# Kernel optimization log

Hardware: AMD Instinct MI355X
Metric: run time of the kernel (lower is better)

The kernel has to match this reference:

```python
import jax, jax.numpy as jnp
import numpy as np

D_MODEL = 256
D_FFN = 1024
N_LEVELS = 4
N_HEADS = 8
N_POINTS = 4
HEAD_DIM = D_MODEL // N_HEADS
SPATIAL = [(128, 128), (64, 64), (32, 32), (16, 16)]
LQ = sum(h * w for h, w in SPATIAL)  # 21760
B = 2


def setup_inputs() -> dict:
    key = jax.random.key(0)
    ks = jax.random.split(key, 24)

    def w(k, shape, s=0.02):
        return (jax.random.normal(k, shape) * s).astype(jnp.float32)

    HLP = N_HEADS * N_LEVELS * N_POINTS
    starts = np.cumsum([0] + [h * w_ for h, w_ in SPATIAL[:-1]])
    return {
        "src": jax.random.normal(ks[0], (B, LQ, D_MODEL), jnp.float32),
        "pos": 0.1 * jax.random.normal(ks[1], (B, LQ, D_MODEL), jnp.float32),
        "reference_points": jax.random.uniform(ks[2], (B, LQ, N_LEVELS, 2), jnp.float32),
        "W_off": w(ks[3], (D_MODEL, HLP * 2)),
        "b_off": w(ks[4], (HLP * 2,), 0.5),
        "W_attn": w(ks[5], (D_MODEL, HLP)),
        "b_attn": jnp.zeros((HLP,), jnp.float32),
        "W_val": w(ks[6], (D_MODEL, D_MODEL)),
        "b_val": jnp.zeros((D_MODEL,), jnp.float32),
        "W_out": w(ks[7], (D_MODEL, D_MODEL)),
        "b_out": jnp.zeros((D_MODEL,), jnp.float32),
        "ln1_g": jnp.ones((D_MODEL,), jnp.float32),
        "ln1_b": jnp.zeros((D_MODEL,), jnp.float32),
        "W1": w(ks[8], (D_MODEL, D_FFN)),
        "b1": jnp.zeros((D_FFN,), jnp.float32),
        "W2": w(ks[9], (D_FFN, D_MODEL)),
        "b2": jnp.zeros((D_MODEL,), jnp.float32),
        "ln2_g": jnp.ones((D_MODEL,), jnp.float32),
        "ln2_b": jnp.zeros((D_MODEL,), jnp.float32),
        "spatial_shapes": np.array(SPATIAL, np.int32),
        "level_start_index": np.array(starts, np.int32),
    }


def _layernorm(x, g, b):
    mu = x.mean(-1, keepdims=True)
    var = ((x - mu) ** 2).mean(-1, keepdims=True)
    return (x - mu) * jax.lax.rsqrt(var + 1e-5) * g + b


def _bilinear_sample(v, x, y, H, W):
    # v: [N, H, W, D]; x, y: [N, Lq, P] pixel coords (align_corners=False, zero pad)
    x0f = jnp.floor(x)
    y0f = jnp.floor(y)
    x0 = x0f.astype(jnp.int32)
    y0 = y0f.astype(jnp.int32)
    wx1 = x - x0f
    wy1 = y - y0f
    wx0 = 1.0 - wx1
    wy0 = 1.0 - wy1
    vf = v.reshape(v.shape[0], H * W, v.shape[-1])

    def gather(xi, yi, wt):
        valid = (xi >= 0) & (xi < W) & (yi >= 0) & (yi < H)
        idx = jnp.clip(yi, 0, H - 1) * W + jnp.clip(xi, 0, W - 1)
        g = jnp.take_along_axis(vf, idx.reshape(idx.shape[0], -1)[..., None], axis=1)
        g = g.reshape(*xi.shape, vf.shape[-1])
        return g * (wt * valid.astype(wt.dtype))[..., None]

    return (gather(x0, y0, wx0 * wy0) + gather(x0 + 1, y0, wx1 * wy0)
            + gather(x0, y0 + 1, wx0 * wy1) + gather(x0 + 1, y0 + 1, wx1 * wy1))


def _ms_deform_attn(query, src, reference_points, W_off, b_off, W_attn, b_attn,
                    W_val, b_val, W_out, b_out, spatial_shapes):
    Bq, Lq, _ = query.shape
    ss = np.asarray(spatial_shapes)
    value = (src @ W_val + b_val).reshape(Bq, Lq, N_HEADS, HEAD_DIM)
    off = (query @ W_off + b_off).reshape(Bq, Lq, N_HEADS, N_LEVELS, N_POINTS, 2)
    attn = (query @ W_attn + b_attn).reshape(Bq, Lq, N_HEADS, N_LEVELS * N_POINTS)
    attn = jax.nn.softmax(attn, axis=-1).reshape(Bq, Lq, N_HEADS, N_LEVELS, N_POINTS)
    # offset normalizer = (W, H) per level
    normalizer = jnp.asarray(ss[:, ::-1].astype(np.float32))  # [L, 2]
    loc = reference_points[:, :, None, :, None, :] + off / normalizer[None, None, None, :, None, :]
    # loc: [B, Lq, M, L, P, 2] normalized in [0,1]
    out = jnp.zeros((Bq, N_HEADS, Lq, HEAD_DIM), query.dtype)
    start = 0
    for lvl in range(N_LEVELS):
        H, W = int(ss[lvl, 0]), int(ss[lvl, 1])
        v = value[:, start:start + H * W]                                 # [B, HW, M, D]
        v = v.transpose(0, 2, 1, 3).reshape(Bq * N_HEADS, H, W, HEAD_DIM)
        l = loc[:, :, :, lvl]                                             # [B, Lq, M, P, 2]
        x = (l[..., 0] * W - 0.5).transpose(0, 2, 1, 3).reshape(Bq * N_HEADS, Lq, N_POINTS)
        y = (l[..., 1] * H - 0.5).transpose(0, 2, 1, 3).reshape(Bq * N_HEADS, Lq, N_POINTS)
        sampled = _bilinear_sample(v, x, y, H, W)                         # [BM, Lq, P, D]
        wgt = attn[:, :, :, lvl].transpose(0, 2, 1, 3).reshape(Bq * N_HEADS, Lq, N_POINTS)
        out = out + (sampled * wgt[..., None]).sum(2).reshape(Bq, N_HEADS, Lq, HEAD_DIM)
        start += H * W
    out = out.transpose(0, 2, 1, 3).reshape(Bq, Lq, D_MODEL)
    return out @ W_out + b_out


def reference(src, pos, reference_points, W_off, b_off, W_attn, b_attn, W_val, b_val,
              W_out, b_out, ln1_g, ln1_b, W1, b1, W2, b2, ln2_g, ln2_b,
              spatial_shapes, level_start_index):
    query = src + pos
    src2 = _ms_deform_attn(query, src, reference_points, W_off, b_off, W_attn, b_attn,
                           W_val, b_val, W_out, b_out, spatial_shapes)
    h = _layernorm(src + src2, ln1_g, ln1_b)
    ffn = jax.nn.relu(h @ W1 + b1) @ W2 + b2
    return _layernorm(h + ffn, ln2_g, ln2_b)
```

## Files before the change

### kernel.cpp

```cpp
#include <hip/hip_runtime.h>

typedef __bf16 bf16x8 __attribute__((ext_vector_type(8)));
typedef float f32x4 __attribute__((ext_vector_type(4)));

static constexpr int TOKS = 43520;
static constexpr int LQN  = 21760;

__device__ __forceinline__ unsigned short f2bf(float f) {
  union { float f; unsigned u; } v; v.f = f;
  return (unsigned short)((v.u + 0x7fffu + ((v.u >> 16) & 1u)) >> 16);
}
__device__ __forceinline__ float bf2f(unsigned short b) {
  union { unsigned u; float f; } v; v.u = ((unsigned)b) << 16; return v.f;
}

__global__ __launch_bounds__(256) void prewt_kernel(
    const float* __restrict__ src, const float* __restrict__ pos,
    unsigned short* __restrict__ srcb, unsigned short* __restrict__ qb,
    const float* __restrict__ W_val, const float* __restrict__ W_off,
    const float* __restrict__ W_attn, const float* __restrict__ W_out,
    const float* __restrict__ W1, const float* __restrict__ W2,
    const float* __restrict__ b_off, const float* __restrict__ b_attn,
    unsigned short* __restrict__ Wt_val, unsigned short* __restrict__ Wt_oa,
    unsigned short* __restrict__ Wt_out,
    unsigned short* __restrict__ Wt_1, unsigned short* __restrict__ Wt_2,
    float* __restrict__ b_oa) {
  const int bid = blockIdx.x;
  if (bid < 10880) {
    int i = bid * 256 + threadIdx.x;
    float4 s = ((const float4*)src)[i], p = ((const float4*)pos)[i];
    ((ushort4*)srcb)[i] = make_ushort4(f2bf(s.x), f2bf(s.y), f2bf(s.z), f2bf(s.w));
    ((ushort4*)qb)[i]   = make_ushort4(f2bf(s.x + p.x), f2bf(s.y + p.y),
                                       f2bf(s.z + p.z), f2bf(s.w + p.w));
    return;
  }
  int gid = (bid - 10880) * 256 + threadIdx.x;
  if (gid >= 754048) return;
  if (gid >= 753664) {
    int i = gid - 753664;
    b_oa[i] = (i < 256) ? b_off[i] : b_attn[i - 256];
    return;
  }
  const float* W; unsigned short* Wt; int idx, K, nsh;
  if (gid < 65536)       { W = W_val;  Wt = Wt_val;          idx = gid;          K = 256;  nsh = 8;  }
  else if (gid < 131072) { W = W_off;  Wt = Wt_oa;           idx = gid - 65536;  K = 256;  nsh = 8;  }
  else if (gid < 163840) { W = W_attn; Wt = Wt_oa + 65536;   idx = gid - 131072; K = 256;  nsh = 7;  }
  else if (gid < 229376) { W = W_out;  Wt = Wt_out;          idx = gid - 163840; K = 256;  nsh = 8;  }
  else if (gid < 491520) { W = W1;     Wt = Wt_1;            idx = gid - 229376; K = 256;  nsh = 10; }
  else                   { W = W2;     Wt = Wt_2;            idx = gid - 491520; K = 1024; nsh = 8;  }
  int k = idx >> nsh, n = idx & ((1 << nsh) - 1);
  Wt[n * K + k] = f2bf(W[idx]);
}

template <int K, int OUTOP>
__device__ __forceinline__ void gemm_body(unsigned short* __restrict__ As,
                                          unsigned short* __restrict__ Bs,
                                          const unsigned short* __restrict__ A,
                                          const unsigned short* __restrict__ Bt,
                                          const float* __restrict__ bias,
                                          const unsigned short* __restrict__ res,
                                          unsigned short* __restrict__ Cp,
                                          int N, int bm, int bn) {
  const int t = threadIdx.x;
  const int wave = t >> 6, lane = t & 63;
  const int wm = (wave & 1) << 6, wn = (wave >> 1) << 6;
  const int lr = lane & 15, lq = lane >> 4;
  const int row0 = t >> 2, cb0 = (t & 3) << 3;
  f32x4 acc[4][4] = {};
  const unsigned short* ga = A  + (size_t)(bm * 128 + row0) * K + cb0;
  const unsigned short* gb = Bt + (size_t)(bn * 128 + row0) * K + cb0;
  const size_t gs = (size_t)64 * K;
  uint4 pa0 = *(const uint4*)ga;
  uint4 pa1 = *(const uint4*)(ga + gs);
  uint4 pb0 = *(const uint4*)gb;
  uint4 pb1 = *(const uint4*)(gb + gs);
  int p = 0;
#pragma unroll 1
  for (int k0 = 0; k0 < K; k0 += 32) {
    unsigned short* Ab = As + p * 5120;
    unsigned short* Bb = Bs + p * 5120;
    *(uint4*)&Ab[row0 * 40 + cb0] = pa0;
    *(uint4*)&Ab[(row0 + 64) * 40 + cb0] = pa1;
    *(uint4*)&Bb[row0 * 40 + cb0] = pb0;
    *(uint4*)&Bb[(row0 + 64) * 40 + cb0] = pb1;
    __syncthreads();
    if (k0 + 32 < K) {
      pa0 = *(const uint4*)(ga + k0 + 32);
      pa1 = *(const uint4*)(ga + gs + k0 + 32);
      pb0 = *(const uint4*)(gb + k0 + 32);
      pb1 = *(const uint4*)(gb + gs + k0 + 32);
    }
    bf16x8 af[4], bfr[4];
#pragma unroll
    for (int i = 0; i < 4; i++) af[i] = *(const bf16x8*)&Ab[(wm + i * 16 + lr) * 40 + lq * 8];
#pragma unroll
    for (int j = 0; j < 4; j++) bfr[j] = *(const bf16x8*)&Bb[(wn + j * 16 + lr) * 40 + lq * 8];
#pragma unroll
    for (int i = 0; i < 4; i++)
#pragma unroll
      for (int j = 0; j < 4; j++)
        acc[i][j] = __builtin_amdgcn_mfma_f32_16x16x32_bf16(af[i], bfr[j], acc[i][j], 0, 0, 0);
    p ^= 1;
  }
  const int rb = bm * 128 + wm + lq * 4;
  const int cbase = bn * 128 + wn + lr;
#pragma unroll
  for (int j = 0; j < 4; j++) {
    const int col = cbase + j * 16;
    const float bv = bias[col];
#pragma unroll
    for (int i = 0; i < 4; i++) {
#pragma unroll
      for (int r = 0; r < 4; r++) {
        float v = acc[i][j][r] + bv;
        size_t o = (size_t)(rb + i * 16 + r) * N + col;
        if (OUTOP == 1) Cp[o] = f2bf(v);
        else if (OUTOP == 2) Cp[o] = f2bf(fmaxf(v, 0.f));
        else Cp[o] = f2bf(v + bf2f(res[o]));
      }
    }
  }
}

__global__ __launch_bounds__(256) void proj_kernel(
    const unsigned short* __restrict__ srcb, const unsigned short* __restrict__ qb,
    const unsigned short* __restrict__ Wt_val, const unsigned short* __restrict__ Wt_oa,
    const float* __restrict__ b_val, const float* __restrict__ b_oa,
    unsigned short* __restrict__ valb, unsigned short* __restrict__ oab) {
  __shared__ unsigned short As[2 * 5120];
  __shared__ unsigned short Bs[2 * 5120];
  const int bn = blockIdx.y;
  if (bn < 2)
    gemm_body<256, 1>(As, Bs, srcb, Wt_val, b_val, nullptr, valb, 256, blockIdx.x, bn);
  else
    gemm_body<256, 1>(As, Bs, qb, Wt_oa, b_oa, nullptr, oab, 384, blockIdx.x, bn - 2);
}

template <int K, int MODE>
__device__ __forceinline__ void big_body(unsigned short* __restrict__ As,
                                         unsigned short* __restrict__ Bs,
                                         const unsigned short* __restrict__ A,
                                         const unsigned short* __restrict__ Bt,
                                         const float* __restrict__ bias,
                                         const unsigned short* __restrict__ res,
                                         const float* __restrict__ gamma,
                                         const float* __restrict__ beta,
                                         void* __restrict__ outp,
                                         int N, int bm, int bn) {
  const int t = threadIdx.x;
  const int wave = t >> 6, lane = t & 63;
  const int wm = (wave & 1) << 6, wn = (wave >> 1) << 7;
  const int lr = lane & 15, lq = lane >> 4;
  const int row0 = t >> 2, cb0 = (t & 3) << 3;
  f32x4 acc[4][8] = {};
  const unsigned short* ga = A  + (size_t)(bm * 128 + row0) * K + cb0;
  const unsigned short* gb = Bt + (size_t)(bn * 256 + row0) * K + cb0;
  const size_t gs = (size_t)64 * K;
  uint4 pa0 = *(const uint4*)ga;
  uint4 pa1 = *(const uint4*)(ga + gs);
  uint4 pb0 = *(const uint4*)gb;
  uint4 pb1 = *(const uint4*)(gb + gs);
  uint4 pb2 = *(const uint4*)(gb + 2 * gs);
  uint4 pb3 = *(const uint4*)(gb + 3 * gs);
  int p = 0;
#pragma unroll 1
  for (int k0 = 0; k0 < K; k0 += 32) {
    unsigned short* Ab = As + p * 5120;
    unsigned short* Bb = Bs + p * 10240;
    *(uint4*)&Ab[row0 * 40 + cb0] = pa0;
    *(uint4*)&Ab[(row0 + 64) * 40 + cb0] = pa1;
    *(uint4*)&Bb[row0 * 40 + cb0] = pb0;
    *(uint4*)&Bb[(row0 + 64) * 40 + cb0] = pb1;
    *(uint4*)&Bb[(row0 + 128) * 40 + cb0] = pb2;
    *(uint4*)&Bb[(row0 + 192) * 40 + cb0] = pb3;
    __syncthreads();
    if (k0 + 32 < K) {
      pa0 = *(const uint4*)(ga + k0 + 32);
      pa1 = *(const uint4*)(ga + gs + k0 + 32);
      pb0 = *(const uint4*)(gb + k0 + 32);
      pb1 = *(const uint4*)(gb + gs + k0 + 32);
      pb2 = *(const uint4*)(gb + 2 * gs + k0 + 32);
      pb3 = *(const uint4*)(gb + 3 * gs + k0 + 32);
    }
    bf16x8 af[4], bfr[8];
#pragma unroll
    for (int i = 0; i < 4; i++) af[i]  = *(const bf16x8*)&Ab[(wm + i * 16 + lr) * 40 + lq * 8];
#pragma unroll
    for (int j = 0; j < 8; j++) bfr[j] = *(const bf16x8*)&Bb[(wn + j * 16 + lr) * 40 + lq * 8];
#pragma unroll
    for (int i = 0; i < 4; i++)
#pragma unroll
      for (int j = 0; j < 8; j++)
        acc[i][j] = __builtin_amdgcn_mfma_f32_16x16x32_bf16(af[i], bfr[j], acc[i][j], 0, 0, 0);
    p ^= 1;
  }
  const int rb = bm * 128 + wm + lq * 4;
  if (MODE == 0) {
    const int cbase = bn * 256 + wn + lr;
#pragma unroll
    for (int j = 0; j < 8; j++) {
      const int col = cbase + j * 16;
      const float bv = bias[col];
#pragma unroll
      for (int i = 0; i < 4; i++)
#pragma unroll
        for (int r = 0; r < 4; r++) {
          float v = acc[i][j][r] + bv;
          ((unsigned short*)outp)[(size_t)(rb + i * 16 + r) * N + col] = f2bf(fmaxf(v, 0.f));
        }
    }
    return;
  }
  __syncthreads();
  float* red = (float*)As;
  const int wnIdx = wave >> 1;
  float vsum[4][4], vsq[4][4];
#pragma unroll
  for (int i = 0; i < 4; i++)
#pragma unroll
    for (int r = 0; r < 4; r++) { vsum[i][r] = 0.f; vsq[i][r] = 0.f; }
#pragma unroll
  for (int j = 0; j < 8; j++) {
    const int col = wn + j * 16 + lr;
    const float bv = bias[col];
#pragma unroll
    for (int i = 0; i < 4; i++)
#pragma unroll
      for (int r = 0; r < 4; r++) {
        const int grow = rb + i * 16 + r;
        float v = acc[i][j][r] + bv + bf2f(res[(size_t)grow * 256 + col]);
        acc[i][j][r] = v;
        vsum[i][r] += v;
        vsq[i][r]  += v * v;
      }
  }
#pragma unroll
  for (int m = 1; m <= 8; m <<= 1)
#pragma unroll
    for (int i = 0; i < 4; i++)
#pragma unroll
      for (int r = 0; r < 4; r++) {
        vsum[i][r] += __shfl_xor(vsum[i][r], m, 64);
        vsq[i][r]  += __shfl_xor(vsq[i][r],  m, 64);
      }
  if (lr == 0) {
#pragma unroll
    for (int i = 0; i < 4; i++)
#pragma unroll
      for (int r = 0; r < 4; r++) {
        const int lrow = wm + i * 16 + lq * 4 + r;
        red[wnIdx * 128 + lrow]       = vsum[i][r];
        red[256 + wnIdx * 128 + lrow] = vsq[i][r];
      }
  }
  __syncthreads();
  float mu[4][4], rstd[4][4];
#pragma unroll
  for (int i = 0; i < 4; i++)
#pragma unroll
    for (int r = 0; r < 4; r++) {
      const int lrow = wm + i * 16 + lq * 4 + r;
      const float ts = vsum[i][r] + red[(1 - wnIdx) * 128 + lrow];
      const float tq = vsq[i][r]  + red[256 + (1 - wnIdx) * 128 + lrow];
      const float m_ = ts * (1.f / 256.f);
      float var = tq * (1.f / 256.f) - m_ * m_;
      mu[i][r] = m_;
      rstd[i][r] = rsqrtf(var + 1e-5f);
    }
#pragma unroll
  for (int j = 0; j < 8; j++) {
    const int col = wn + j * 16 + lr;
    const float gg = gamma[col], bb = beta[col];
#pragma unroll
    for (int i = 0; i < 4; i++)
#pragma unroll
      for (int r = 0; r < 4; r++) {
        const int grow = rb + i * 16 + r;
        const float y = (acc[i][j][r] - mu[i][r]) * rstd[i][r] * gg + bb;
        if (MODE == 1) ((unsigned short*)outp)[(size_t)grow * 256 + col] = f2bf(y);
        else           ((float*)outp)[(size_t)grow * 256 + col] = y;
      }
  }
}

__global__ __launch_bounds__(256, 2) void out_ln_kernel(
    const unsigned short* __restrict__ A, const unsigned short* __restrict__ Bt,
    const float* __restrict__ bias, const unsigned short* __restrict__ res,
    const float* __restrict__ gamma, const float* __restrict__ beta,
    unsigned short* __restrict__ C) {
  __shared__ unsigned short As[2 * 5120];
  __shared__ unsigned short Bs[2 * 10240];
  big_body<256, 1>(As, Bs, A, Bt, bias, res, gamma, beta, C, 256, blockIdx.x, 0);
}

__global__ __launch_bounds__(256, 2) void ffn1_kernel(
    const unsigned short* __restrict__ A, const unsigned short* __restrict__ Bt,
    const float* __restrict__ bias, unsigned short* __restrict__ C) {
  __shared__ unsigned short As[2 * 5120];
  __shared__ unsigned short Bs[2 * 10240];
  big_body<256, 0>(As, Bs, A, Bt, bias, nullptr, nullptr, nullptr, C, 1024,
                   blockIdx.x, blockIdx.y);
}

__global__ __launch_bounds__(256, 2) void ffn2_ln_kernel(
    const unsigned short* __restrict__ A, const unsigned short* __restrict__ Bt,
    const float* __restrict__ bias, const unsigned short* __restrict__ res,
    const float* __restrict__ gamma, const float* __restrict__ beta,
    float* __restrict__ C) {
  __shared__ unsigned short As[2 * 5120];
  __shared__ unsigned short Bs[2 * 10240];
  big_body<1024, 2>(As, Bs, A, Bt, bias, res, gamma, beta, C, 256, blockIdx.x, 0);
}

__device__ __forceinline__ void fma8(uint4 v, float w, float* a) {
  const unsigned uu[4] = {v.x, v.y, v.z, v.w};
#pragma unroll
  for (int i = 0; i < 4; i++) {
    union { unsigned u; float f; } lo, hi;
    lo.u = uu[i] << 16;
    hi.u = uu[i] & 0xffff0000u;
    a[2 * i]     += w * lo.f;
    a[2 * i + 1] += w * hi.f;
  }
}

__global__ __launch_bounds__(256) void deform_kernel(const unsigned short* __restrict__ valb,
                                                     const unsigned short* __restrict__ oab,
                                                     const float* __restrict__ refp,
                                                     unsigned short* __restrict__ outb) {
  __shared__ float4 sW[8][8][17];
  __shared__ int4   sI[8][8][17];
  const int t = threadIdx.x;
  const int bid = blockIdx.x;
  const int nb = (bid & 7) * 680 + (bid >> 3);
  const int tok0 = nb * 8;

  {
    const int g = t >> 5, h = (t >> 2) & 7, l = t & 3;
    const int tok = tok0 + g;
    const unsigned short* lg = oab + (size_t)tok * 384 + 256 + h * 16;
    uint4 lv0 = ((const uint4*)lg)[0];
    uint4 lv1 = ((const uint4*)lg)[1];
    const unsigned lw[8] = {lv0.x, lv0.y, lv0.z, lv0.w, lv1.x, lv1.y, lv1.z, lv1.w};
    float w[16];
#pragma unroll
    for (int i = 0; i < 8; i++) {
      union { unsigned u; float f; } lo, hi;
      lo.u = lw[i] << 16; hi.u = lw[i] & 0xffff0000u;
      w[2 * i] = lo.f; w[2 * i + 1] = hi.f;
    }
    float mx = -1e30f;
#pragma unroll
    for (int i = 0; i < 16; i++) mx = fmaxf(mx, w[i]);
    float s = 0.f;
#pragma unroll
    for (int i = 0; i < 16; i++) { w[i] = __expf(w[i] - mx); s += w[i]; }
    const float inv = 1.f / s;
    uint4 ov = *(const uint4*)(oab + (size_t)tok * 384 + h * 32 + l * 8);
    const unsigned owv[4] = {ov.x, ov.y, ov.z, ov.w};
    float off[8];
#pragma unroll
    for (int i = 0; i < 4; i++) {
      union { unsigned u; float f; } lo, hi;
      lo.u = owv[i] << 16; hi.u = owv[i] & 0xffff0000u;
      off[2 * i] = lo.f; off[2 * i + 1] = hi.f;
    }
    const float* rp = refp + (size_t)tok * 8 + l * 2;
    const int S = 128 >> l;
    const float Sf = (float)S;
    const float rx = rp[0] * Sf - 0.5f;
    const float ry = rp[1] * Sf - 0.5f;
#pragma unroll
    for (int p = 0; p < 4; p++) {
      const int idx = l * 4 + p;
      const float x = rx + off[p * 2 + 0];
      const float y = ry + off[p * 2 + 1];
      const float aw = w[idx] * inv;
      const float x0f = floorf(x), y0f = floorf(y);
      const int x0 = (int)x0f, y0 = (int)y0f;
      const float fx = x - x0f, fy = y - y0f;
      const bool xin0 = (x0 >= 0) & (x0 < S), xin1 = (x0 + 1 >= 0) & (x0 + 1 < S);
      const bool yin0 = (y0 >= 0) & (y0 < S), yin1 = (y0 + 1 >= 0) & (y0 + 1 < S);
      const int xc0 = min(max(x0, 0), S - 1), xc1 = min(max(x0 + 1, 0), S - 1);
      const int yc0 = min(max(y0, 0), S - 1), yc1 = min(max(y0 + 1, 0), S - 1);
      sW[g][h][idx] = make_float4(aw * (1.f - fx) * (1.f - fy) * (float)(xin0 & yin0),
                                  aw * fx * (1.f - fy)         * (float)(xin1 & yin0),
                                  aw * (1.f - fx) * fy         * (float)(xin0 & yin1),
                                  aw * fx * fy                 * (float)(xin1 & yin1));
      sI[g][h][idx] = make_int4((yc0 * S + xc0) << 9, (yc0 * S + xc1) << 9,
                                (yc1 * S + xc0) << 9, (yc1 * S + xc1) << 9);
    }
  }
  __syncthreads();

  const int g = t >> 5, h = (t >> 2) & 7, dc = t & 3;
  const int tok = tok0 + g;
  const int b = tok / LQN;
  float acc[8] = {0.f, 0.f, 0.f, 0.f, 0.f, 0.f, 0.f, 0.f};
  const int ST[4] = {0, 16384, 20480, 21504};
#pragma unroll
  for (int l = 0; l < 4; l++) {
    const char* vbc = (const char*)(valb + ((size_t)(b * LQN + ST[l])) * 256 + h * 32 + dc * 8);
#pragma unroll
    for (int p = 0; p < 4; p++) {
      float4 W4 = sW[g][h][l * 4 + p];
      int4   I4 = sI[g][h][l * 4 + p];
      uint4 v00 = *(const uint4*)(vbc + I4.x);
      uint4 v10 = *(const uint4*)(vbc + I4.y);
      uint4 v01 = *(const uint4*)(vbc + I4.z);
      uint4 v11 = *(const uint4*)(vbc + I4.w);
      fma8(v00, W4.x, acc);
      fma8(v10, W4.y, acc);
      fma8(v01, W4.z, acc);
      fma8(v11, W4.w, acc);
    }
  }
  unsigned o[4];
#pragma unroll
  for (int i = 0; i < 4; i++)
    o[i] = (unsigned)f2bf(acc[2 * i]) | ((unsigned)f2bf(acc[2 * i + 1]) << 16);
  *(uint4*)(outb + (size_t)tok * 256 + h * 32 + dc * 8) = make_uint4(o[0], o[1], o[2], o[3]);
}

extern "C" void kernel_launch(void* const* d_in, const int* in_sizes, int n_in,
                              void* d_out, int out_size, void* d_ws, size_t ws_size,
                              hipStream_t stream) {
  (void)in_sizes; (void)n_in; (void)out_size; (void)ws_size;
  const float* src    = (const float*)d_in[0];
  const float* pos    = (const float*)d_in[1];
  const float* refp   = (const float*)d_in[2];
  const float* W_off  = (const float*)d_in[3];
  const float* b_off  = (const float*)d_in[4];
  const float* W_attn = (const float*)d_in[5];
  const float* b_attn = (const float*)d_in[6];
  const float* W_val  = (const float*)d_in[7];
  const float* b_val  = (const float*)d_in[8];
  const float* W_out  = (const float*)d_in[9];
  const float* b_out  = (const float*)d_in[10];
  const float* ln1_g  = (const float*)d_in[11];
  const float* ln1_b  = (const float*)d_in[12];
  const float* W1     = (const float*)d_in[13];
  const float* b1     = (const float*)d_in[14];
  const float* W2     = (const float*)d_in[15];
  const float* b2     = (const float*)d_in[16];
  const float* ln2_g  = (const float*)d_in[17];
  const float* ln2_b  = (const float*)d_in[18];

  char* ws = (char*)d_ws;
  unsigned short* Wt_val = (unsigned short*)ws;
  unsigned short* Wt_oa  = Wt_val + 65536;
  unsigned short* Wt_out = Wt_oa + 98304;
  unsigned short* Wt_1   = Wt_out + 65536;
  unsigned short* Wt_2   = Wt_1 + 262144;
  float*          b_oa   = (float*)(Wt_2 + 262144);
  const size_t WPOOL = 2u * 1024 * 1024;

  const size_t SZ_bf = (size_t)TOKS * 256 * 2;
  const size_t SZ_oa = (size_t)TOKS * 384 * 2;

  unsigned short* srcb = (unsigned short*)(ws + WPOOL);
  unsigned short* qb   = (unsigned short*)(ws + WPOOL + SZ_bf);
  unsigned short* valb = (unsigned short*)(ws + WPOOL + 2 * SZ_bf);
  unsigned short* oab  = (unsigned short*)(ws + WPOOL + 3 * SZ_bf);
  unsigned short* h_bf = (unsigned short*)(ws + WPOOL + 3 * SZ_bf + SZ_oa);
  unsigned short* hb   = (unsigned short*)(ws + WPOOL + 3 * SZ_bf + SZ_oa + SZ_bf);
  unsigned short* attnoutb = qb;

  prewt_kernel<<<13826, 256, 0, stream>>>(src, pos, srcb, qb,
                                          W_val, W_off, W_attn, W_out, W1, W2, b_off, b_attn,
                                          Wt_val, Wt_oa, Wt_out, Wt_1, Wt_2, b_oa);

  proj_kernel<<<dim3(340, 5), 256, 0, stream>>>(srcb, qb, Wt_val, Wt_oa, b_val, b_oa,
                                                valb, oab);

  deform_kernel<<<TOKS / 8, 256, 0, stream>>>(valb, oab, refp, attnoutb);

  out_ln_kernel<<<340, 256, 0, stream>>>(attnoutb, Wt_out, b_out, srcb, ln1_g, ln1_b, h_bf);

  ffn1_kernel<<<dim3(340, 4), 256, 0, stream>>>(h_bf, Wt_1, b1, hb);

  ffn2_ln_kernel<<<340, 256, 0, stream>>>(hb, Wt_2, b2, h_bf, ln2_g, ln2_b, (float*)d_out);
}
```

Before: 437.0 us.

## Stage GEMM tiles with direct global-to-LDS loads and drop row padding

Replaces the register-staged global loads and LDS stores in both GEMM bodies with global_load_lds (direct DMA into shared memory). The next tile's load is issued into the other buffer while MFMAs run on the current one, with a barrier at the end of each iteration. The LDS row pitch drops from 40 to 32 elements because direct loads need a contiguous layout. This frees VGPRs and removes the ds_write instructions, but the unpadded layout may cause LDS bank conflicts on the fragment reads. The sync placement also relies on the compiler inserting proper vmcnt waits before the barrier.

```diff
diff --git a/kernel.cpp b/kernel.cpp
--- a/kernel.cpp
+++ b/kernel.cpp
@@ -12,6 +12,12 @@
 }
 __device__ __forceinline__ float bf2f(unsigned short b) {
   union { unsigned u; float f; } v; v.u = ((unsigned)b) << 16; return v.f;
+}
+
+__device__ __forceinline__ void gload16(const unsigned short* g, unsigned short* l) {
+  __builtin_amdgcn_global_load_lds((const __attribute__((address_space(1))) unsigned int*)g,
+                                   (__attribute__((address_space(3))) unsigned int*)l,
+                                   16, 0, 0);
 }
 
 __global__ __launch_bounds__(256) void prewt_kernel(
@@ -65,41 +71,45 @@
   const int wave = t >> 6, lane = t & 63;
   const int wm = (wave & 1) << 6, wn = (wave >> 1) << 6;
   const int lr = lane & 15, lq = lane >> 4;
-  const int row0 = t >> 2, cb0 = (t & 3) << 3;
+  const int srow = t >> 2;
+  const unsigned short* gsA = A  + (size_t)(bm * 128 + srow) * K + (t & 3) * 8;
+  const unsigned short* gsB = Bt + (size_t)(bn * 128 + srow) * K + (t & 3) * 8;
+  const size_t gstep = (size_t)64 * K;
   f32x4 acc[4][4] = {};
-  const unsigned short* ga = A  + (size_t)(bm * 128 + row0) * K + cb0;
-  const unsigned short* gb = Bt + (size_t)(bn * 128 + row0) * K + cb0;
-  const size_t gs = (size_t)64 * K;
-  uint4 pa0 = *(const uint4*)ga;
-  uint4 pa1 = *(const uint4*)(ga + gs);
-  uint4 pb0 = *(const uint4*)gb;
-  uint4 pb1 = *(const uint4*)(gb + gs);
+
+  {
+    unsigned short* Ad = As + wave * 512;
+    unsigned short* Bd = Bs + wave * 512;
+    gload16(gsA,         Ad);
+    gload16(gsA + gstep, Ad + 2048);
+    gload16(gsB,         Bd);
+    gload16(gsB + gstep, Bd + 2048);
+  }
+  __syncthreads();
   int p = 0;
-#pragma unroll 1
+#pragma unroll 2
   for (int k0 = 0; k0 < K; k0 += 32) {
-    unsigned short* Ab = As + p * 5120;
-    unsigned short* Bb = Bs + p * 5120;
-    *(uint4*)&Ab[row0 * 40 + cb0] = pa0;
-    *(uint4*)&Ab[(row0 + 64) * 40 + cb0] = pa1;
-    *(uint4*)&Bb[row0 * 40 + cb0] = pb0;
-    *(uint4*)&Bb[(row0 + 64) * 40 + cb0] = pb1;
-    __syncthreads();
     if (k0 + 32 < K) {
-      pa0 = *(const uint4*)(ga + k0 + 32);
-      pa1 = *(const uint4*)(ga + gs + k0 + 32);
-      pb0 = *(const uint4*)(gb + k0 + 32);
-      pb1 = *(const uint4*)(gb + gs + k0 + 32);
-    }
+      unsigned short* Ad = As + (p ^ 1) * 4096 + wave * 512;
+      unsigned short* Bd = Bs + (p ^ 1) * 4096 + wave * 512;
+      gload16(gsA + k0 + 32,         Ad);
+      gload16(gsA + gstep + k0 + 32, Ad + 2048);
+      gload16(gsB + k0 + 32,         Bd);
+      gload16(gsB + gstep + k0 + 32, Bd + 2048);
+    }
+    const unsigned short* Ab = As + p * 4096;
+    const unsigned short* Bb = Bs + p * 4096;
     bf16x8 af[4], bfr[4];
 #pragma unroll
-    for (int i = 0; i < 4; i++) af[i] = *(const bf16x8*)&Ab[(wm + i * 16 + lr) * 40 + lq * 8];
-#pragma unroll
-    for (int j = 0; j < 4; j++) bfr[j] = *(const bf16x8*)&Bb[(wn + j * 16 + lr) * 40 + lq * 8];
+    for (int i = 0; i < 4; i++) af[i]  = *(const bf16x8*)&Ab[(wm + i * 16 + lr) * 32 + lq * 8];
+#pragma unroll
+    for (int j = 0; j < 4; j++) bfr[j] = *(const bf16x8*)&Bb[(wn + j * 16 + lr) * 32 + lq * 8];
 #pragma unroll
     for (int i = 0; i < 4; i++)
 #pragma unroll
       for (int j = 0; j < 4; j++)
         acc[i][j] = __builtin_amdgcn_mfma_f32_16x16x32_bf16(af[i], bfr[j], acc[i][j], 0, 0, 0);
+    __syncthreads();
     p ^= 1;
   }
   const int rb = bm * 128 + wm + lq * 4;
@@ -127,8 +137,8 @@
     const unsigned short* __restrict__ Wt_val, const unsigned short* __restrict__ Wt_oa,
     const float* __restrict__ b_val, const float* __restrict__ b_oa,
     unsigned short* __restrict__ valb, unsigned short* __restrict__ oab) {
-  __shared__ unsigned short As[2 * 5120];
-  __shared__ unsigned short Bs[2 * 5120];
+  __shared__ unsigned short As[2 * 4096];
+  __shared__ unsigned short Bs[2 * 4096];
   const int bn = blockIdx.y;
   if (bn < 2)
     gemm_body<256, 1>(As, Bs, srcb, Wt_val, b_val, nullptr, valb, 256, blockIdx.x, bn);
@@ -151,47 +161,49 @@
   const int wave = t >> 6, lane = t & 63;
   const int wm = (wave & 1) << 6, wn = (wave >> 1) << 7;
   const int lr = lane & 15, lq = lane >> 4;
-  const int row0 = t >> 2, cb0 = (t & 3) << 3;
+  const int srow = t >> 2;
+  const unsigned short* gsA = A  + (size_t)(bm * 128 + srow) * K + (t & 3) * 8;
+  const unsigned short* gsB = Bt + (size_t)(bn * 256 + srow) * K + (t & 3) * 8;
+  const size_t gstep = (size_t)64 * K;
   f32x4 acc[4][8] = {};
-  const unsigned short* ga = A  + (size_t)(bm * 128 + row0) * K + cb0;
-  const unsigned short* gb = Bt + (size_t)(bn * 256 + row0) * K + cb0;
-  const size_t gs = (size_t)64 * K;
-  uint4 pa0 = *(const uint4*)ga;
-  uint4 pa1 = *(const uint4*)(ga + gs);
-  uint4 pb0 = *(const uint4*)gb;
-  uint4 pb1 = *(const uint4*)(gb + gs);
-  uint4 pb2 = *(const uint4*)(gb + 2 * gs);
-  uint4 pb3 = *(const uint4*)(gb + 3 * gs);
+
+  {
+    unsigned short* Ad = As + wave * 512;
+    unsigned short* Bd = Bs + wave * 512;
+    gload16(gsA,             Ad);
+    gload16(gsA + gstep,     Ad + 2048);
+    gload16(gsB,             Bd);
+    gload16(gsB + gstep,     Bd + 2048);
+    gload16(gsB + 2 * gstep, Bd + 4096);
+    gload16(gsB + 3 * gstep, Bd + 6144);
+  }
+  __syncthreads();
   int p = 0;
-#pragma unroll 1
+#pragma unroll 2
   for (int k0 = 0; k0 < K; k0 += 32) {
-    unsigned short* Ab = As + p * 5120;
-    unsigned short* Bb = Bs + p * 10240;
-    *(uint4*)&Ab[row0 * 40 + cb0] = pa0;
-    *(uint4*)&Ab[(row0 + 64) * 40 + cb0] = pa1;
-    *(uint4*)&Bb[row0 * 40 + cb0] = pb0;
-    *(uint4*)&Bb[(row0 + 64) * 40 + cb0] = pb1;
-    *(uint4*)&Bb[(row0 + 128) * 40 + cb0] = pb2;
-    *(uint4*)&Bb[(row0 + 192) * 40 + cb0] = pb3;
-    __syncthreads();
     if (k0 + 32 < K) {
-      pa0 = *(const uint4*)(ga + k0 + 32);
-      pa1 = *(const uint4*)(ga + gs + k0 + 32);
-      pb0 = *(const uint4*)(gb + k0 + 32);
-      pb1 = *(const uint4*)(gb + gs + k0 + 32);
-      pb2 = *(const uint4*)(gb + 2 * gs + k0 + 32);
-      pb3 = *(const uint4*)(gb + 3 * gs + k0 + 32);
-    }
+      unsigned short* Ad = As + (p ^ 1) * 4096 + wave * 512;
+      unsigned short* Bd = Bs + (p ^ 1) * 8192 + wave * 512;
+      gload16(gsA + k0 + 32,             Ad);
+      gload16(gsA + gstep + k0 + 32,     Ad + 2048);
+      gload16(gsB + k0 + 32,             Bd);
+      gload16(gsB + gstep + k0 + 32,     Bd + 2048);
+      gload16(gsB + 2 * gstep + k0 + 32, Bd + 4096);
+      gload16(gsB + 3 * gstep + k0 + 32, Bd + 6144);
+    }
+    const unsigned short* Ab = As + p * 4096;
+    const unsigned short* Bb = Bs + p * 8192;
     bf16x8 af[4], bfr[8];
 #pragma unroll
-    for (int i = 0; i < 4; i++) af[i]  = *(const bf16x8*)&Ab[(wm + i * 16 + lr) * 40 + lq * 8];
-#pragma unroll
-    for (int j = 0; j < 8; j++) bfr[j] = *(const bf16x8*)&Bb[(wn + j * 16 + lr) * 40 + lq * 8];
+    for (int i = 0; i < 4; i++) af[i]  = *(const bf16x8*)&Ab[(wm + i * 16 + lr) * 32 + lq * 8];
+#pragma unroll
+    for (int j = 0; j < 8; j++) bfr[j] = *(const bf16x8*)&Bb[(wn + j * 16 + lr) * 32 + lq * 8];
 #pragma unroll
     for (int i = 0; i < 4; i++)
 #pragma unroll
       for (int j = 0; j < 8; j++)
         acc[i][j] = __builtin_amdgcn_mfma_f32_16x16x32_bf16(af[i], bfr[j], acc[i][j], 0, 0, 0);
+    __syncthreads();
     p ^= 1;
   }
   const int rb = bm * 128 + wm + lq * 4;
@@ -288,16 +300,16 @@
     const float* __restrict__ bias, const unsigned short* __restrict__ res,
     const float* __restrict__ gamma, const float* __restrict__ beta,
     unsigned short* __restrict__ C) {
-  __shared__ unsigned short As[2 * 5120];
-  __shared__ unsigned short Bs[2 * 10240];
+  __shared__ unsigned short As[2 * 4096];
+  __shared__ unsigned short Bs[2 * 8192];
   big_body<256, 1>(As, Bs, A, Bt, bias, res, gamma, beta, C, 256, blockIdx.x, 0);
 }
 
 __global__ __launch_bounds__(256, 2) void ffn1_kernel(
     const unsigned short* __restrict__ A, const unsigned short* __restrict__ Bt,
     const float* __restrict__ bias, unsigned short* __restrict__ C) {
-  __shared__ unsigned short As[2 * 5120];
-  __shared__ unsigned short Bs[2 * 10240];
+  __shared__ unsigned short As[2 * 4096];
+  __shared__ unsigned short Bs[2 * 8192];
   big_body<256, 0>(As, Bs, A, Bt, bias, nullptr, nullptr, nullptr, C, 1024,
                    blockIdx.x, blockIdx.y);
 }
@@ -307,8 +319,8 @@
     const float* __restrict__ bias, const unsigned short* __restrict__ res,
     const float* __restrict__ gamma, const float* __restrict__ beta,
     float* __restrict__ C) {
-  __shared__ unsigned short As[2 * 5120];
-  __shared__ unsigned short Bs[2 * 10240];
+  __shared__ unsigned short As[2 * 4096];
+  __shared__ unsigned short Bs[2 * 8192];
   big_body<1024, 2>(As, Bs, A, Bt, bias, res, gamma, beta, C, 256, blockIdx.x, 0);
 }
 
```

Measured after the change: 447.0 us. 2.3% more time.

## Fuse FFN up-projection, ReLU, down-projection and LayerNorm into one kernel

Applied to the files above, without the earlier changes.

Replaces the separate FFN1 and FFN2+LN kernels with one kernel that keeps a 64-row tile of h in shared memory. It computes the 1024-wide hidden activation in 128-column chunks, applies ReLU into shared memory and accumulates the down-projection in registers before the residual add and LayerNorm. This removes the global write and read of the 43520x1024 bf16 hidden tensor and one launch. In exchange, weights are read straight from global memory per wave with no shared-memory staging, and the small 64-row tiles reduce per-block reuse.

```diff
diff --git a/kernel.cpp b/kernel.cpp
--- a/kernel.cpp
+++ b/kernel.cpp
@@ -293,23 +293,163 @@
   big_body<256, 1>(As, Bs, A, Bt, bias, res, gamma, beta, C, 256, blockIdx.x, 0);
 }
 
-__global__ __launch_bounds__(256, 2) void ffn1_kernel(
-    const unsigned short* __restrict__ A, const unsigned short* __restrict__ Bt,
-    const float* __restrict__ bias, unsigned short* __restrict__ C) {
-  __shared__ unsigned short As[2 * 5120];
-  __shared__ unsigned short Bs[2 * 10240];
-  big_body<256, 0>(As, Bs, A, Bt, bias, nullptr, nullptr, nullptr, C, 1024,
-                   blockIdx.x, blockIdx.y);
-}
-
-__global__ __launch_bounds__(256, 2) void ffn2_ln_kernel(
-    const unsigned short* __restrict__ A, const unsigned short* __restrict__ Bt,
-    const float* __restrict__ bias, const unsigned short* __restrict__ res,
+__global__ __launch_bounds__(256, 2) void ffn_fused_kernel(
+    const unsigned short* __restrict__ h,
+    const unsigned short* __restrict__ W1t,
+    const unsigned short* __restrict__ W2t,
+    const float* __restrict__ b1, const float* __restrict__ b2,
     const float* __restrict__ gamma, const float* __restrict__ beta,
-    float* __restrict__ C) {
-  __shared__ unsigned short As[2 * 5120];
-  __shared__ unsigned short Bs[2 * 10240];
-  big_body<1024, 2>(As, Bs, A, Bt, bias, res, gamma, beta, C, 256, blockIdx.x, 0);
+    float* __restrict__ out) {
+  __shared__ unsigned short Ah[64 * 264];
+  __shared__ unsigned short Hc[64 * 136];
+  __shared__ float red[2][4][64];
+  const int t = threadIdx.x;
+  const int w = t >> 6, lane = t & 63;
+  const int lr = lane & 15, lq = lane >> 4;
+  const size_t rowbase = (size_t)blockIdx.x * 64;
+
+  {
+    const uint4* gsrc = (const uint4*)(h + rowbase * 256);
+#pragma unroll
+    for (int u = 0; u < 8; u++) {
+      const int idx = u * 256 + t;
+      const int row = idx >> 5, c8 = idx & 31;
+      *(uint4*)&Ah[row * 264 + c8 * 8] = gsrc[idx];
+    }
+  }
+  __syncthreads();
+
+  f32x4 acc2[4][4] = {};
+  const int c1base = w * 32;
+#pragma unroll 1
+  for (int c2 = 0; c2 < 8; c2++) {
+    f32x4 acc1[4][2] = {};
+    const size_t w1r0 = (size_t)(c2 * 128 + c1base + lr) * 256;
+    const size_t w1r1 = (size_t)(c2 * 128 + c1base + 16 + lr) * 256;
+    bf16x8 bfn0 = *(const bf16x8*)&W1t[w1r0 + lq * 8];
+    bf16x8 bfn1 = *(const bf16x8*)&W1t[w1r1 + lq * 8];
+#pragma unroll 1
+    for (int ks = 0; ks < 8; ks++) {
+      const int k0 = ks * 32;
+      bf16x8 b0 = bfn0, b1v = bfn1;
+      if (ks < 7) {
+        bfn0 = *(const bf16x8*)&W1t[w1r0 + k0 + 32 + lq * 8];
+        bfn1 = *(const bf16x8*)&W1t[w1r1 + k0 + 32 + lq * 8];
+      }
+      bf16x8 af[4];
+#pragma unroll
+      for (int i = 0; i < 4; i++)
+        af[i] = *(const bf16x8*)&Ah[(i * 16 + lr) * 264 + k0 + lq * 8];
+#pragma unroll
+      for (int i = 0; i < 4; i++) {
+        acc1[i][0] = __builtin_amdgcn_mfma_f32_16x16x32_bf16(af[i], b0,  acc1[i][0], 0, 0, 0);
+        acc1[i][1] = __builtin_amdgcn_mfma_f32_16x16x32_bf16(af[i], b1v, acc1[i][1], 0, 0, 0);
+      }
+    }
+    __syncthreads();
+#pragma unroll
+    for (int j = 0; j < 2; j++) {
+      const int colc = c1base + j * 16 + lr;
+      const float bv = b1[c2 * 128 + colc];
+#pragma unroll
+      for (int i = 0; i < 4; i++)
+#pragma unroll
+        for (int r = 0; r < 4; r++)
+          Hc[(i * 16 + lq * 4 + r) * 136 + colc] = f2bf(fmaxf(acc1[i][j][r] + bv, 0.f));
+    }
+    __syncthreads();
+    const size_t w2base = (size_t)(w * 64 + lr) * 1024 + c2 * 128;
+    bf16x8 cfn0 = *(const bf16x8*)&W2t[w2base + lq * 8];
+    bf16x8 cfn1 = *(const bf16x8*)&W2t[w2base + 16 * 1024 + lq * 8];
+    bf16x8 cfn2 = *(const bf16x8*)&W2t[w2base + 32 * 1024 + lq * 8];
+    bf16x8 cfn3 = *(const bf16x8*)&W2t[w2base + 48 * 1024 + lq * 8];
+#pragma unroll 1
+    for (int ks = 0; ks < 4; ks++) {
+      const int k2 = ks * 32;
+      bf16x8 c0 = cfn0, c1 = cfn1, c2v = cfn2, c3 = cfn3;
+      if (ks < 3) {
+        cfn0 = *(const bf16x8*)&W2t[w2base + k2 + 32 + lq * 8];
+        cfn1 = *(const bf16x8*)&W2t[w2base + 16 * 1024 + k2 + 32 + lq * 8];
+        cfn2 = *(const bf16x8*)&W2t[w2base + 32 * 1024 + k2 + 32 + lq * 8];
+        cfn3 = *(const bf16x8*)&W2t[w2base + 48 * 1024 + k2 + 32 + lq * 8];
+      }
+      bf16x8 af2[4];
+#pragma unroll
+      for (int i = 0; i < 4; i++)
+        af2[i] = *(const bf16x8*)&Hc[(i * 16 + lr) * 136 + k2 + lq * 8];
+#pragma unroll
+      for (int i = 0; i < 4; i++) {
+        acc2[i][0] = __builtin_amdgcn_mfma_f32_16x16x32_bf16(af2[i], c0,  acc2[i][0], 0, 0, 0);
+        acc2[i][1] = __builtin_amdgcn_mfma_f32_16x16x32_bf16(af2[i], c1,  acc2[i][1], 0, 0, 0);
+        acc2[i][2] = __builtin_amdgcn_mfma_f32_16x16x32_bf16(af2[i], c2v, acc2[i][2], 0, 0, 0);
+        acc2[i][3] = __builtin_amdgcn_mfma_f32_16x16x32_bf16(af2[i], c3,  acc2[i][3], 0, 0, 0);
+      }
+    }
+  }
+  float vsum[4][4], vsq[4][4];
+#pragma unroll
+  for (int i = 0; i < 4; i++)
+#pragma unroll
+    for (int r = 0; r < 4; r++) { vsum[i][r] = 0.f; vsq[i][r] = 0.f; }
+#pragma unroll
+  for (int j = 0; j < 4; j++) {
+    const int col = w * 64 + j * 16 + lr;
+    const float bv = b2[col];
+#pragma unroll
+    for (int i = 0; i < 4; i++)
+#pragma unroll
+      for (int r = 0; r < 4; r++) {
+        const int row = i * 16 + lq * 4 + r;
+        float v = acc2[i][j][r] + bv + bf2f(Ah[row * 264 + col]);
+        acc2[i][j][r] = v;
+        vsum[i][r] += v;
+        vsq[i][r]  += v * v;
+      }
+  }
+#pragma unroll
+  for (int m = 1; m <= 8; m <<= 1)
+#pragma unroll
+    for (int i = 0; i < 4; i++)
+#pragma unroll
+      for (int r = 0; r < 4; r++) {
+        vsum[i][r] += __shfl_xor(vsum[i][r], m, 64);
+        vsq[i][r]  += __shfl_xor(vsq[i][r],  m, 64);
+      }
+  if (lr == 0) {
+#pragma unroll
+    for (int i = 0; i < 4; i++)
+#pragma unroll
+      for (int r = 0; r < 4; r++) {
+        const int row = i * 16 + lq * 4 + r;
+        red[0][w][row] = vsum[i][r];
+        red[1][w][row] = vsq[i][r];
+      }
+  }
+  __syncthreads();
+  float mu[4][4], rstd[4][4];
+#pragma unroll
+  for (int i = 0; i < 4; i++)
+#pragma unroll
+    for (int r = 0; r < 4; r++) {
+      const int row = i * 16 + lq * 4 + r;
+      const float ts = red[0][0][row] + red[0][1][row] + red[0][2][row] + red[0][3][row];
+      const float tq = red[1][0][row] + red[1][1][row] + red[1][2][row] + red[1][3][row];
+      const float m_ = ts * (1.f / 256.f);
+      mu[i][r] = m_;
+      rstd[i][r] = rsqrtf(tq * (1.f / 256.f) - m_ * m_ + 1e-5f);
+    }
+#pragma unroll
+  for (int j = 0; j < 4; j++) {
+    const int col = w * 64 + j * 16 + lr;
+    const float gg = gamma[col], bb = beta[col];
+#pragma unroll
+    for (int i = 0; i < 4; i++)
+#pragma unroll
+      for (int r = 0; r < 4; r++) {
+        const int row = i * 16 + lq * 4 + r;
+        out[(rowbase + row) * 256 + col] = (acc2[i][j][r] - mu[i][r]) * rstd[i][r] * gg + bb;
+      }
+  }
 }
 
 __device__ __forceinline__ void fma8(uint4 v, float w, float* a) {
@@ -463,7 +603,6 @@
   unsigned short* valb = (unsigned short*)(ws + WPOOL + 2 * SZ_bf);
   unsigned short* oab  = (unsigned short*)(ws + WPOOL + 3 * SZ_bf);
   unsigned short* h_bf = (unsigned short*)(ws + WPOOL + 3 * SZ_bf + SZ_oa);
-  unsigned short* hb   = (unsigned short*)(ws + WPOOL + 3 * SZ_bf + SZ_oa + SZ_bf);
   unsigned short* attnoutb = qb;
 
   prewt_kernel<<<13826, 256, 0, stream>>>(src, pos, srcb, qb,
@@ -477,7 +616,6 @@
 
   out_ln_kernel<<<340, 256, 0, stream>>>(attnoutb, Wt_out, b_out, srcb, ln1_g, ln1_b, h_bf);
 
-  ffn1_kernel<<<dim3(340, 4), 256, 0, stream>>>(h_bf, Wt_1, b1, hb);
-
-  ffn2_ln_kernel<<<340, 256, 0, stream>>>(hb, Wt_2, b2, h_bf, ln2_g, ln2_b, (float*)d_out);
-}
+  ffn_fused_kernel<<<680, 256, 0, stream>>>(h_bf, Wt_1, Wt_2, b1, b2, ln2_g, ln2_b,
+                                            (float*)d_out);
+}
```

New measurement: 435.6 us. About the same (-0.3%).
